# Performance work log

Measured on AMD Instinct MI355X. Metric: run time of the kernel, lower is better.

## Reference

```python
import jax, jax.numpy as jnp
import numpy as np
from jax import lax

C = 128
HEADS = 8
WS = 8
HIDDEN = C * 4


def _ln2d(x, w, b, eps=1e-6):
    # channel-first LayerNorm over dim 1 of [B,C,H,W]
    u = x.mean(axis=1, keepdims=True)
    s = ((x - u) ** 2).mean(axis=1, keepdims=True)
    xh = (x - u) / jnp.sqrt(s + eps)
    return w[None, :, None, None] * xh + b[None, :, None, None]


def _partition(x, ws):
    # [B,C,H,W] -> [B*nW, ws*ws, C]
    B, C_, H, W = x.shape
    x = x.transpose(0, 2, 3, 1)  # BHWC
    x = x.reshape(B, H // ws, ws, W // ws, ws, C_)
    x = x.transpose(0, 1, 3, 2, 4, 5)
    return x.reshape(-1, ws * ws, C_)


def _reverse(x, ws, H, W, B):
    # [B*nW, ws*ws, C] -> [B,C,H,W]
    C_ = x.shape[-1]
    x = x.reshape(B, H // ws, W // ws, ws, ws, C_)
    x = x.transpose(0, 1, 3, 2, 4, 5).reshape(B, H, W, C_)
    return x.transpose(0, 3, 1, 2)


def setup_inputs() -> dict:
    key = jax.random.key(0)
    ks = jax.random.split(key, 16)
    B, H, W = 4, 256, 256
    inp = {
        "x": jax.random.normal(ks[0], (B, C, H, W), jnp.float32),
        "l0": jax.random.uniform(ks[1], (B, 1, H, W), jnp.float32),
        "norm1_w": jnp.ones((C,), jnp.float32),
        "norm1_b": jnp.zeros((C,), jnp.float32),
        "norm2_w": jnp.ones((C,), jnp.float32),
        "norm2_b": jnp.zeros((C,), jnp.float32),
        "qkv_w": jax.random.normal(ks[2], (3 * C, C), jnp.float32) * (1.0 / np.sqrt(C)),
        "gate_w": jax.random.normal(ks[3], (C,), jnp.float32),
        "gate_b": jnp.zeros((C,), jnp.float32),
        "proj_w": jax.random.normal(ks[4], (C, C), jnp.float32) * (1.0 / np.sqrt(C)),
        "proj_b": jnp.zeros((C,), jnp.float32),
        "ffn_w1": jax.random.normal(ks[5], (HIDDEN, C), jnp.float32) * (1.0 / np.sqrt(C)),
        "ffn_b1": jnp.zeros((HIDDEN,), jnp.float32),
        "ffn_dw": jax.random.normal(ks[6], (HIDDEN, 1, 3, 3), jnp.float32) * (1.0 / 3.0),
        "ffn_dwb": jnp.zeros((HIDDEN,), jnp.float32),
        "ffn_w2": jax.random.normal(ks[7], (C, HIDDEN), jnp.float32) * (1.0 / np.sqrt(HIDDEN)),
        "ffn_b2": jnp.zeros((C,), jnp.float32),
    }
    return inp


def reference(x, l0, norm1_w, norm1_b, norm2_w, norm2_b, qkv_w, gate_w, gate_b,
              proj_w, proj_b, ffn_w1, ffn_b1, ffn_dw, ffn_dwb, ffn_w2, ffn_b2):
    B, C_, H, W = x.shape
    ws = WS
    # H,W chosen divisible by ws -> no padding branch
    head_dim = C_ // HEADS
    scale = head_dim ** -0.5

    shortcut = x
    xn = _ln2d(x, norm1_w, norm1_b)
    qkv = jnp.einsum("oc,bchw->bohw", qkv_w, xn)
    q, k, v = jnp.split(qkv, 3, axis=1)

    # illumination gate (l0 already at [H,W]; bilinear resize to same size is identity)
    gate = jax.nn.sigmoid(l0 * gate_w[None, :, None, None] + gate_b[None, :, None, None])
    q = q * gate

    q = _partition(q, ws)  # [Bw, ws*ws, C]
    k = _partition(k, ws)
    v = _partition(v, ws)
    Bw, N, _ = q.shape
    q = q.reshape(Bw, N, HEADS, head_dim)
    k = k.reshape(Bw, N, HEADS, head_dim)
    v = v.reshape(Bw, N, HEADS, head_dim)

    attn = jnp.einsum("bqhd,bkhd->bhqk", q, k) * scale
    attn = jax.nn.softmax(attn, axis=-1)
    out = jnp.einsum("bhqk,bkhd->bqhd", attn, v).reshape(Bw, N, C_)
    out = _reverse(out, ws, H, W, B)

    out = jnp.einsum("oc,bchw->bohw", proj_w, out) + proj_b[None, :, None, None]
    out = out + shortcut

    # FFN: 1x1 -> GELU -> depthwise 3x3 -> GELU -> 1x1
    h = _ln2d(out, norm2_w, norm2_b)
    h = jnp.einsum("oc,bchw->bohw", ffn_w1, h) + ffn_b1[None, :, None, None]
    h = jax.nn.gelu(h, approximate=False)
    h = lax.conv_general_dilated(h, ffn_dw, window_strides=(1, 1), padding="SAME",
                                 dimension_numbers=("NCHW", "OIHW", "NCHW"),
                                 feature_group_count=HIDDEN)
    h = h + ffn_dwb[None, :, None, None]
    h = jax.nn.gelu(h, approximate=False)
    h = jnp.einsum("oc,bchw->bohw", ffn_w2, h) + ffn_b2[None, :, None, None]
    return out + h
```

## Files before the change

### kernel.cpp

```cpp
#include <hip/hip_runtime.h>
#include <hip/hip_bf16.h>

#define HW   65536
#define CHW  (128*65536)
#define QKV_OZ  33554432u
#define QKV_H   1048576u
#define QKV_WIN 1024u

typedef __attribute__((ext_vector_type(8))) short bf16x8;
typedef __attribute__((ext_vector_type(4))) short bf16x4;
typedef __attribute__((ext_vector_type(4))) float f32x4;

__device__ __forceinline__ float geluf(float v){
    float u = 0.7978845608028654f * v * (1.f + 0.044715f*v*v);
    float e = __expf(2.f*u);
    float th = 1.f - 2.f/(e+1.f);
    return 0.5f*v*(1.f+th);
}

__device__ __forceinline__ float sigmoidf_(float z){
    return 1.f / (1.f + __expf(-z));
}

__device__ __forceinline__ float bf2f(short s){
    return __uint_as_float(((unsigned)(unsigned short)s) << 16);
}

__global__ __launch_bounds__(256) void k_cvt(
    const float* __restrict__ src, __hip_bfloat16* __restrict__ dst, int n)
{
    int i = blockIdx.x*256 + threadIdx.x;
    if (i < n) dst[i] = __float2bfloat16(src[i]);
}

__global__ __launch_bounds__(512,2) void k_ln_qkv_mfma(
    const float* __restrict__ x, const float* __restrict__ l0,
    const float* __restrict__ n1w, const float* __restrict__ n1b,
    const __hip_bfloat16* __restrict__ qkvw, const float* __restrict__ gate_w,
    const float* __restrict__ gate_b, __hip_bfloat16* __restrict__ qkvb)
{
    __shared__ short sxb[128*130];
    __shared__ float sp1[512], sp2[512];
    const int t = threadIdx.x;
    const int lane = t & 63, w = t >> 6;
    const int l15 = lane & 15, q4 = (lane >> 4)*4, ko = (lane >> 4)*8;
    const int mq = w & 3, phalf = w >> 2;
    const int pbase = blockIdx.x * 128;
    const int b = pbase >> 16;
    const int hw0 = pbase & 65535;
    const int x0 = hw0 & 255;
    const int y  = hw0 >> 8;
    const int wy = y >> 3, ty = y & 7;
    const int pxs = t & 127, cq = t >> 7;
    const float* xb = x + (size_t)b*CHW + (size_t)cq*32*HW + hw0 + pxs;
    unsigned* srow = (unsigned*)sxb + pxs*65 + cq*16;

    float s1 = 0.f, s2 = 0.f;
    #pragma unroll
    for (int j = 0; j < 16; ++j) {
        float v0 = xb[(size_t)(2*j)*HW];
        float v1 = xb[(size_t)(2*j+1)*HW];
        s1 += v0 + v1; s2 += v0*v0 + v1*v1;
        __hip_bfloat162 pk = __float22bfloat162_rn(make_float2(v0, v1));
        srow[j] = *(unsigned*)&pk;
    }
    sp1[cq*128 + pxs] = s1;
    sp2[cq*128 + pxs] = s2;
    __syncthreads();
    const float s1t = sp1[pxs] + sp1[128+pxs] + sp1[256+pxs] + sp1[384+pxs];
    const float s2t = sp2[pxs] + sp2[128+pxs] + sp2[256+pxs] + sp2[384+pxs];
    const float mean = s1t * 0.0078125f;
    const float rstd = rsqrtf(s2t*0.0078125f - mean*mean + 1e-6f);
    #pragma unroll
    for (int j = 0; j < 16; ++j) {
        unsigned u = srow[j];
        float v0 = __uint_as_float(u << 16);
        float v1 = __uint_as_float(u & 0xffff0000u);
        const int c = cq*32 + 2*j;
        v0 = (v0 - mean)*rstd*n1w[c]   + n1b[c];
        v1 = (v1 - mean)*rstd*n1w[c+1] + n1b[c+1];
        __hip_bfloat162 pk = __float22bfloat162_rn(make_float2(v0, v1));
        srow[j] = *(unsigned*)&pk;
    }
    __syncthreads();

    float lv[4];
    #pragma unroll
    for (int nt = 0; nt < 4; ++nt)
        lv[nt] = l0[(size_t)b*HW + hw0 + phalf*64 + nt*16 + l15];

    unsigned toff[4];
    #pragma unroll
    for (int nt = 0; nt < 4; ++nt) {
        const int xg = x0 + phalf*64 + nt*16 + l15;
        toff[nt] = (unsigned)((wy*32 + (xg >> 3))*1024 + (ty*8 + (xg & 7))*16);
    }

    const short* wq = (const short*)qkvw;
    for (int oz = 0; oz < 3; ++oz) {
        f32x4 acc[2][4];
        #pragma unroll
        for (int mt = 0; mt < 2; ++mt)
            #pragma unroll
            for (int nt = 0; nt < 4; ++nt)
                acc[mt][nt] = (f32x4){0.f,0.f,0.f,0.f};
        #pragma unroll
        for (int kc = 0; kc < 4; ++kc) {
            bf16x8 bfrag[4];
            #pragma unroll
            for (int nt = 0; nt < 4; ++nt) {
                const int px = phalf*64 + nt*16 + l15;
                bfrag[nt] = *(const bf16x8*)(sxb + px*130 + kc*32 + ko);
            }
            #pragma unroll
            for (int mt = 0; mt < 2; ++mt) {
                const int m = oz*128 + mq*32 + mt*16 + l15;
                bf16x8 af = *(const bf16x8*)(wq + m*128 + kc*32 + ko);
                #pragma unroll
                for (int nt = 0; nt < 4; ++nt)
                    acc[mt][nt] = __builtin_amdgcn_mfma_f32_16x16x32_bf16(af, bfrag[nt], acc[mt][nt], 0, 0, 0);
            }
        }
        __hip_bfloat16* ob = qkvb + (size_t)oz*QKV_OZ + (size_t)b*8*QKV_H;
        #pragma unroll
        for (int mt = 0; mt < 2; ++mt) {
            const int h = mq*2 + mt;
            #pragma unroll
            for (int nt = 0; nt < 4; ++nt) {
                float v0 = acc[mt][nt][0], v1 = acc[mt][nt][1];
                float v2 = acc[mt][nt][2], v3 = acc[mt][nt][3];
                if (oz == 0) {
                    const int o = h*16 + q4;
                    v0 *= sigmoidf_(lv[nt]*gate_w[o]   + gate_b[o]);
                    v1 *= sigmoidf_(lv[nt]*gate_w[o+1] + gate_b[o+1]);
                    v2 *= sigmoidf_(lv[nt]*gate_w[o+2] + gate_b[o+2]);
                    v3 *= sigmoidf_(lv[nt]*gate_w[o+3] + gate_b[o+3]);
                }
                __hip_bfloat162 p0 = __float22bfloat162_rn(make_float2(v0, v1));
                __hip_bfloat162 p1 = __float22bfloat162_rn(make_float2(v2, v3));
                uint2 st;
                st.x = *(unsigned*)&p0;
                st.y = *(unsigned*)&p1;
                *(uint2*)(ob + (size_t)h*QKV_H + toff[nt] + q4) = st;
            }
        }
    }
}

__global__ __launch_bounds__(256) void k_attn(
    const __hip_bfloat16* __restrict__ qkv, unsigned* __restrict__ apack)
{
    __shared__ short vt[4][16*72];
    __shared__ short pt[4][64*68];
    const int t = threadIdx.x;
    const int l = t & 63, w = t >> 6;
    const int c = l & 15, g = l >> 4;
    const int id = blockIdx.x*4 + w;
    const int b = id >> 13;
    const int head = (id >> 10) & 7;
    const int wi = id & 1023;
    const __hip_bfloat16* qp = qkv + ((size_t)(b*8 + head))*QKV_H + (size_t)wi*QKV_WIN;
    const __hip_bfloat16* kp = qp + QKV_OZ;
    const __hip_bfloat16* vp = qp + 2u*QKV_OZ;

    bf16x8 v0 = *(const bf16x8*)(vp + l*16);
    bf16x8 v1 = *(const bf16x8*)(vp + l*16 + 8);
    short* vtw = &vt[w][0];
    #pragma unroll
    for (int d = 0; d < 8; ++d) vtw[d*72 + l] = v0[d];
    #pragma unroll
    for (int d = 0; d < 8; ++d) vtw[(8+d)*72 + l] = v1[d];

    bf16x8 kf[4], qf[4];
    #pragma unroll
    for (int mj = 0; mj < 4; ++mj) {
        if (g < 2) {
            kf[mj] = *(const bf16x8*)(kp + (mj*16 + c)*16 + g*8);
            qf[mj] = *(const bf16x8*)(qp + (mj*16 + c)*16 + g*8);
        } else {
            kf[mj] = (bf16x8){0,0,0,0,0,0,0,0};
            qf[mj] = (bf16x8){0,0,0,0,0,0,0,0};
        }
    }
    f32x4 st[4][4];
    #pragma unroll
    for (int mj = 0; mj < 4; ++mj)
        #pragma unroll
        for (int ni = 0; ni < 4; ++ni)
            st[mj][ni] = (f32x4){0.f,0.f,0.f,0.f};
    #pragma unroll
    for (int mj = 0; mj < 4; ++mj)
        #pragma unroll
        for (int ni = 0; ni < 4; ++ni)
            st[mj][ni] = __builtin_amdgcn_mfma_f32_16x16x32_bf16(kf[mj], qf[ni], st[mj][ni], 0, 0, 0);

    float rs[4];
    bf16x4 pa[4][4], pb[4][4];
    #pragma unroll
    for (int ni = 0; ni < 4; ++ni) {
        float mx = -1e30f;
        #pragma unroll
        for (int mj = 0; mj < 4; ++mj)
            #pragma unroll
            for (int r = 0; r < 4; ++r)
                mx = fmaxf(mx, st[mj][ni][r]);
        mx = fmaxf(mx, __shfl_xor(mx, 16));
        mx = fmaxf(mx, __shfl_xor(mx, 32));
        mx *= 0.25f;
        float sum = 0.f;
        #pragma unroll
        for (int mj = 0; mj < 4; ++mj) {
            float p[4], lo[4];
            #pragma unroll
            for (int r = 0; r < 4; ++r) {
                p[r] = __expf(st[mj][ni][r]*0.25f - mx);
                sum += p[r];
            }
            __hip_bfloat162 h0 = __float22bfloat162_rn(make_float2(p[0], p[1]));
            __hip_bfloat162 h1 = __float22bfloat162_rn(make_float2(p[2], p[3]));
            union { unsigned u[2]; bf16x4 v; } hi;
            hi.u[0] = *(unsigned*)&h0; hi.u[1] = *(unsigned*)&h1;
            pa[mj][ni] = hi.v;
            #pragma unroll
            for (int r = 0; r < 4; ++r) lo[r] = p[r] - bf2f(hi.v[r]);
            __hip_bfloat162 g0 = __float22bfloat162_rn(make_float2(lo[0], lo[1]));
            __hip_bfloat162 g1 = __float22bfloat162_rn(make_float2(lo[2], lo[3]));
            union { unsigned u[2]; bf16x4 v; } lw;
            lw.u[0] = *(unsigned*)&g0; lw.u[1] = *(unsigned*)&g1;
            pb[mj][ni] = lw.v;
        }
        sum += __shfl_xor(sum, 16);
        sum += __shfl_xor(sum, 32);
        rs[ni] = 1.f / sum;
    }

    short* ptw = &pt[w][0];
    f32x4 oc[4];
    #pragma unroll
    for (int ni = 0; ni < 4; ++ni) oc[ni] = (f32x4){0.f,0.f,0.f,0.f};
    bf16x8 vf[2];
    #pragma unroll
    for (int kb = 0; kb < 2; ++kb)
        vf[kb] = *(const bf16x8*)(vtw + c*72 + kb*32 + g*8);

    #pragma unroll
    for (int mj = 0; mj < 4; ++mj)
        #pragma unroll
        for (int ni = 0; ni < 4; ++ni)
            *(bf16x4*)(ptw + (ni*16 + c)*68 + mj*16 + g*4) = pa[mj][ni];
    __syncthreads();
    #pragma unroll
    for (int kb = 0; kb < 2; ++kb)
        #pragma unroll
        for (int ni = 0; ni < 4; ++ni) {
            bf16x8 pf = *(const bf16x8*)(ptw + (ni*16 + c)*68 + kb*32 + g*8);
            oc[ni] = __builtin_amdgcn_mfma_f32_16x16x32_bf16(vf[kb], pf, oc[ni], 0, 0, 0);
        }
    __syncthreads();
    #pragma unroll
    for (int mj = 0; mj < 4; ++mj)
        #pragma unroll
        for (int ni = 0; ni < 4; ++ni)
            *(bf16x4*)(ptw + (ni*16 + c)*68 + mj*16 + g*4) = pb[mj][ni];
    __syncthreads();
    #pragma unroll
    for (int kb = 0; kb < 2; ++kb)
        #pragma unroll
        for (int ni = 0; ni < 4; ++ni) {
            bf16x8 pf = *(const bf16x8*)(ptw + (ni*16 + c)*68 + kb*32 + g*8);
            oc[ni] = __builtin_amdgcn_mfma_f32_16x16x32_bf16(vf[kb], pf, oc[ni], 0, 0, 0);
        }

    const int wy = wi >> 5, wx = wi & 31;
    unsigned* ob = apack + (size_t)b*64*HW + (size_t)(head*8 + g*2)*HW
                 + (size_t)(wy*8)*256 + wx*8;
    #pragma unroll
    for (int ni = 0; ni < 4; ++ni) {
        const int tok = ni*16 + c;
        const int hw = (tok >> 3)*256 + (tok & 7);
        __hip_bfloat162 p0 = __float22bfloat162_rn(make_float2(oc[ni][0]*rs[ni], oc[ni][1]*rs[ni]));
        __hip_bfloat162 p1 = __float22bfloat162_rn(make_float2(oc[ni][2]*rs[ni], oc[ni][3]*rs[ni]));
        ob[hw]            = *(unsigned*)&p0;
        ob[(size_t)HW+hw] = *(unsigned*)&p1;
    }
}

__global__ __launch_bounds__(256,3) void k_proj_mfma(
    const float* __restrict__ x, const unsigned* __restrict__ apack,
    const __hip_bfloat16* __restrict__ projw,
    const float* __restrict__ proj_b, float* __restrict__ out)
{
    __shared__ short sxb[128*130];
    const int t = threadIdx.x;
    const int lane = t & 63, w = t >> 6;
    const int l15 = lane & 15, q4 = (lane >> 4)*4, ko = (lane >> 4)*8;
    const int mhalf = w & 1, phalf = w >> 1;
    const int pbase = blockIdx.x * 128;
    const int b = pbase >> 16;
    const int hw0 = pbase & 65535;
    const int pxs = t & 127, chalf = t >> 7;
    const unsigned* hsrc = apack + (size_t)b*64*HW + (size_t)chalf*32*HW + hw0 + pxs;
    unsigned* sdst = (unsigned*)sxb + pxs*65 + chalf*32;
    #pragma unroll
    for (int c = 0; c < 32; ++c)
        sdst[c] = hsrc[(size_t)c*HW];
    __syncthreads();
    f32x4 acc[4][4];
    #pragma unroll
    for (int mt = 0; mt < 4; ++mt)
        #pragma unroll
        for (int nt = 0; nt < 4; ++nt)
            acc[mt][nt] = (f32x4){0.f,0.f,0.f,0.f};
    const short* wp = (const short*)projw;
    #pragma unroll
    for (int kc = 0; kc < 4; ++kc) {
        bf16x8 bfrag[4];
        #pragma unroll
        for (int nt = 0; nt < 4; ++nt) {
            const int px = phalf*64 + nt*16 + l15;
            bfrag[nt] = *(const bf16x8*)(sxb + px*130 + kc*32 + ko);
        }
        #pragma unroll
        for (int mt = 0; mt < 4; ++mt) {
            const int m = mhalf*64 + mt*16 + l15;
            bf16x8 af = *(const bf16x8*)(wp + m*128 + kc*32 + ko);
            #pragma unroll
            for (int nt = 0; nt < 4; ++nt)
                acc[mt][nt] = __builtin_amdgcn_mfma_f32_16x16x32_bf16(af, bfrag[nt], acc[mt][nt], 0, 0, 0);
        }
    }
    const float* xb = x + (size_t)b*CHW + hw0;
    float* ob = out + (size_t)b*CHW + hw0;
    #pragma unroll
    for (int mt = 0; mt < 4; ++mt)
        #pragma unroll
        for (int nt = 0; nt < 4; ++nt) {
            const int px = phalf*64 + nt*16 + l15;
            #pragma unroll
            for (int r = 0; r < 4; ++r) {
                const int o = mhalf*64 + mt*16 + q4 + r;
                ob[(size_t)o*HW + px] = acc[mt][nt][r] + proj_b[o] + xb[(size_t)o*HW + px];
            }
        }
}

__global__ __launch_bounds__(256,3) void k_ffn1_mfma(
    const float* __restrict__ outb2, const float* __restrict__ n2w, const float* __restrict__ n2b,
    const __hip_bfloat16* __restrict__ w1, const float* __restrict__ b1,
    __hip_bfloat16* __restrict__ h1s)
{
    __shared__ short sxb[128*130];
    __shared__ float sp1[256], sp2[256];
    const int t = threadIdx.x;
    const int lane = t & 63, w = t >> 6;
    const int l15 = lane & 15, q4 = (lane >> 4)*4, ko = (lane >> 4)*8;
    const int mhalf = w & 1, phalf = w >> 1;
    const int pbase = blockIdx.x * 128;
    const int b = pbase >> 16;
    const int hw0 = pbase & 65535;
    const int pxs = t & 127, chalf = t >> 7;
    const float* xb = outb2 + (size_t)b*CHW + (size_t)chalf*64*HW + hw0 + pxs;
    unsigned* srow = (unsigned*)sxb + pxs*65 + chalf*32;
    float s1 = 0.f, s2 = 0.f;
    #pragma unroll 8
    for (int j = 0; j < 32; ++j) {
        float v0 = xb[(size_t)(2*j)*HW];
        float v1 = xb[(size_t)(2*j+1)*HW];
        s1 += v0 + v1; s2 += v0*v0 + v1*v1;
        __hip_bfloat162 pk = __float22bfloat162_rn(make_float2(v0, v1));
        srow[j] = *(unsigned*)&pk;
    }
    sp1[chalf*128 + pxs] = s1;
    sp2[chalf*128 + pxs] = s2;
    __syncthreads();
    const float s1t = sp1[pxs] + sp1[128 + pxs];
    const float s2t = sp2[pxs] + sp2[128 + pxs];
    const float mean = s1t * 0.0078125f;
    const float rstd = rsqrtf(s2t*0.0078125f - mean*mean + 1e-6f);
    #pragma unroll 8
    for (int j = 0; j < 32; ++j) {
        unsigned u = srow[j];
        float v0 = __uint_as_float(u << 16);
        float v1 = __uint_as_float(u & 0xffff0000u);
        const int c = chalf*64 + 2*j;
        v0 = (v0 - mean)*rstd*n2w[c]   + n2b[c];
        v1 = (v1 - mean)*rstd*n2w[c+1] + n2b[c+1];
        __hip_bfloat162 pk = __float22bfloat162_rn(make_float2(v0, v1));
        srow[j] = *(unsigned*)&pk;
    }
    __syncthreads();
    const short* w1s = (const short*)w1;
    __hip_bfloat16* hb = h1s + (size_t)b*512*HW + hw0;
    for (int mc = 0; mc < 4; ++mc) {
        f32x4 acc[4][4];
        #pragma unroll
        for (int mt = 0; mt < 4; ++mt)
            #pragma unroll
            for (int nt = 0; nt < 4; ++nt)
                acc[mt][nt] = (f32x4){0.f,0.f,0.f,0.f};
        #pragma unroll
        for (int kc = 0; kc < 4; ++kc) {
            bf16x8 bfrag[4];
            #pragma unroll
            for (int nt = 0; nt < 4; ++nt) {
                const int px = phalf*64 + nt*16 + l15;
                bfrag[nt] = *(const bf16x8*)(sxb + px*130 + kc*32 + ko);
            }
            #pragma unroll
            for (int mt = 0; mt < 4; ++mt) {
                const int m = mc*128 + mhalf*64 + mt*16 + l15;
                bf16x8 af = *(const bf16x8*)(w1s + m*128 + kc*32 + ko);
                #pragma unroll
                for (int nt = 0; nt < 4; ++nt)
                    acc[mt][nt] = __builtin_amdgcn_mfma_f32_16x16x32_bf16(af, bfrag[nt], acc[mt][nt], 0, 0, 0);
            }
        }
        #pragma unroll
        for (int mt = 0; mt < 4; ++mt)
            #pragma unroll
            for (int nt = 0; nt < 4; ++nt) {
                const int px = phalf*64 + nt*16 + l15;
                #pragma unroll
                for (int r = 0; r < 4; ++r) {
                    const int o = mc*128 + mhalf*64 + mt*16 + q4 + r;
                    const float v = geluf(acc[mt][nt][r] + b1[o]);
                    hb[(size_t)o*HW + px] = __float2bfloat16(v);
                }
            }
    }
}

__global__ __launch_bounds__(256) void k_dwconv(
    const __hip_bfloat16* __restrict__ h1s,
    unsigned* __restrict__ h2u,
    const float* __restrict__ dwf, const float* __restrict__ dwb)
{
    __shared__ short sh[2*18*260];
    const int t = threadIdx.x;
    const int blk = blockIdx.x;
    const int b   = blk >> 12;
    const int rem = blk & 4095;
    const int rb = rem & 15;
    const int cp = rem >> 4;
    const int row0 = rb * 16;
    const __hip_bfloat16* h1b = h1s + (size_t)b*512*HW;
    #pragma unroll
    for (int ch = 0; ch < 2; ++ch) {
        const __hip_bfloat16* src = h1b + (size_t)(cp*2 + ch)*HW;
        #pragma unroll
        for (int i = 0; i < 9; ++i) {
            const int idx = t + i*256;
            const int r = idx >> 7;
            const int u = idx & 127;
            const int y = row0 - 1 + r;
            unsigned v = 0u;
            if ((unsigned)y < 256u) v = *(const unsigned*)(src + (size_t)y*256 + u*2);
            *(unsigned*)(&sh[ch*4680 + r*260 + 2 + u*2]) = v;
        }
    }
    if (t < 72) {
        const int ch = t / 36, q = t - ch*36;
        const int r = q >> 1;
        sh[ch*4680 + r*260 + ((q & 1) ? 258 : 1)] = 0;
    }
    __syncthreads();
    float wt[2][9], bs[2];
    #pragma unroll
    for (int ch = 0; ch < 2; ++ch) {
        const float* dwc = dwf + (size_t)(cp*2 + ch)*9;
        #pragma unroll
        for (int k = 0; k < 9; ++k) wt[ch][k] = dwc[k];
        bs[ch] = dwb[cp*2 + ch];
    }
    const int xp = (t & 127) * 2;
    const int rh = t >> 7;
    unsigned* h2b = h2u + (size_t)b*256*HW;
    #pragma unroll
    for (int r = 0; r < 8; ++r) {
        const int orow = rh*8 + r;
        const int y = row0 + orow;
        float res[2][2];
        #pragma unroll
        for (int ch = 0; ch < 2; ++ch) {
            const short* base = sh + ch*4680 + orow*260 + xp + 1;
            float a[3][4];
            #pragma unroll
            for (int dy = 0; dy < 3; ++dy)
                #pragma unroll
                for (int k = 0; k < 4; ++k)
                    a[dy][k] = __uint_as_float((unsigned)(unsigned short)base[dy*260 + k] << 16);
            #pragma unroll
            for (int xj = 0; xj < 2; ++xj) {
                float s = bs[ch];
                #pragma unroll
                for (int dy = 0; dy < 3; ++dy)
                    #pragma unroll
                    for (int dx = 0; dx < 3; ++dx)
                        s = fmaf(a[dy][xj+dx], wt[ch][dy*3+dx], s);
                res[ch][xj] = geluf(s);
            }
        }
        __hip_bfloat162 pk0 = __float22bfloat162_rn(make_float2(res[0][0], res[1][0]));
        __hip_bfloat162 pk1 = __float22bfloat162_rn(make_float2(res[0][1], res[1][1]));
        uint2 st;
        st.x = *(unsigned*)&pk0;
        st.y = *(unsigned*)&pk1;
        *(uint2*)(h2b + (size_t)cp*HW + (size_t)y*256 + xp) = st;
    }
}

__global__ __launch_bounds__(256,3) void k_ffn2g(
    const unsigned* __restrict__ h2u, const __hip_bfloat16* __restrict__ w2b,
    const float* __restrict__ b2, float* __restrict__ outb2)
{
    __shared__ short sxb[128*130];
    const int t = threadIdx.x;
    const int lane = t & 63, w = t >> 6;
    const int l15 = lane & 15, q4 = (lane >> 4)*4, ko = (lane >> 4)*8;
    const int mhalf = w & 1, phalf = w >> 1;
    const int pbase = blockIdx.x * 128;
    const int b = pbase >> 16;
    const int hw0 = pbase & 65535;
    const int pxs = t & 127;
    const int chalf = t >> 7;
    const unsigned* h2b = h2u + (size_t)b*256*HW;
    f32x4 acc[4][4];
    #pragma unroll
    for (int mt = 0; mt < 4; ++mt)
        #pragma unroll
        for (int nt = 0; nt < 4; ++nt)
            acc[mt][nt] = (f32x4){0.f,0.f,0.f,0.f};
    const short* w2s = (const short*)w2b;
    for (int k4 = 0; k4 < 4; ++k4) {
        if (k4) __syncthreads();
        const unsigned* hsrc = h2b + (size_t)(k4*64 + chalf*32)*HW + hw0 + pxs;
        unsigned* sdst = (unsigned*)sxb + pxs*65 + chalf*32;
        #pragma unroll
        for (int c = 0; c < 32; ++c)
            sdst[c] = hsrc[(size_t)c*HW];
        __syncthreads();
        #pragma unroll
        for (int kc = 0; kc < 4; ++kc) {
            bf16x8 bfrag[4];
            #pragma unroll
            for (int nt = 0; nt < 4; ++nt) {
                const int px = phalf*64 + nt*16 + l15;
                bfrag[nt] = *(const bf16x8*)(sxb + px*130 + kc*32 + ko);
            }
            #pragma unroll
            for (int mt = 0; mt < 4; ++mt) {
                const int m = mhalf*64 + mt*16 + l15;
                bf16x8 af = *(const bf16x8*)(w2s + (size_t)m*512 + k4*128 + kc*32 + ko);
                #pragma unroll
                for (int nt = 0; nt < 4; ++nt)
                    acc[mt][nt] = __builtin_amdgcn_mfma_f32_16x16x32_bf16(af, bfrag[nt], acc[mt][nt], 0, 0, 0);
            }
        }
    }
    float* ob = outb2 + (size_t)b*CHW;
    #pragma unroll
    for (int mt = 0; mt < 4; ++mt)
        #pragma unroll
        for (int nt = 0; nt < 4; ++nt) {
            const int px = hw0 + phalf*64 + nt*16 + l15;
            #pragma unroll
            for (int r = 0; r < 4; ++r) {
                const int o = mhalf*64 + mt*16 + q4 + r;
                ob[(size_t)o*HW + px] = acc[mt][nt][r] + b2[o] + ob[(size_t)o*HW + px];
            }
        }
}

extern "C" void kernel_launch(void* const* d_in, const int* in_sizes, int n_in,
                              void* d_out, int out_size, void* d_ws, size_t ws_size,
                              hipStream_t stream) {
    const float* x      = (const float*)d_in[0];
    const float* l0     = (const float*)d_in[1];
    const float* n1w    = (const float*)d_in[2];
    const float* n1b    = (const float*)d_in[3];
    const float* n2w    = (const float*)d_in[4];
    const float* n2b    = (const float*)d_in[5];
    const float* qkv_w  = (const float*)d_in[6];
    const float* gate_w = (const float*)d_in[7];
    const float* gate_b = (const float*)d_in[8];
    const float* proj_w = (const float*)d_in[9];
    const float* proj_b = (const float*)d_in[10];
    const float* ffn_w1 = (const float*)d_in[11];
    const float* ffn_b1 = (const float*)d_in[12];
    const float* ffn_dw = (const float*)d_in[13];
    const float* ffn_dwb= (const float*)d_in[14];
    const float* ffn_w2 = (const float*)d_in[15];
    const float* ffn_b2 = (const float*)d_in[16];

    float* out = (float*)d_out;
    __hip_bfloat16* qkvb = (__hip_bfloat16*)d_ws;
    unsigned* apack      = (unsigned*)((char*)d_ws + 201326592);
    __hip_bfloat16* h1s  = (__hip_bfloat16*)d_ws;
    unsigned* h2u        = (unsigned*)((char*)d_ws + 134217728);
    char* wbase = (char*)d_ws + 268435456;
    __hip_bfloat16* qkvw_b = (__hip_bfloat16*)(wbase);
    __hip_bfloat16* projw_b= (__hip_bfloat16*)(wbase + 98304);
    __hip_bfloat16* w1b    = (__hip_bfloat16*)(wbase + 131072);
    __hip_bfloat16* w2b    = (__hip_bfloat16*)(wbase + 262144);

    k_cvt<<<dim3(192), dim3(256), 0, stream>>>(qkv_w, qkvw_b, 49152);
    k_cvt<<<dim3(64),  dim3(256), 0, stream>>>(proj_w, projw_b, 16384);
    k_cvt<<<dim3(256), dim3(256), 0, stream>>>(ffn_w1, w1b, 65536);
    k_cvt<<<dim3(256), dim3(256), 0, stream>>>(ffn_w2, w2b, 65536);

    k_ln_qkv_mfma<<<dim3(2048), dim3(512), 0, stream>>>(x, l0, n1w, n1b, qkvw_b, gate_w, gate_b, qkvb);
    k_attn       <<<dim3(8192), dim3(256), 0, stream>>>(qkvb, apack);
    k_proj_mfma  <<<dim3(2048), dim3(256), 0, stream>>>(x, apack, projw_b, proj_b, out);
    for (int b2 = 0; b2 < 2; ++b2) {
        float* outp = out + (size_t)b2*2*CHW;
        k_ffn1_mfma<<<dim3(1024), dim3(256), 0, stream>>>(outp, n2w, n2b, w1b, ffn_b1, h1s);
        k_dwconv   <<<dim3(8192), dim3(256), 0, stream>>>(h1s, h2u, ffn_dw, ffn_dwb);
        k_ffn2g    <<<dim3(1024), dim3(256), 0, stream>>>(h2u, w2b, ffn_b2, outp);
    }
}
```

Baseline: 1.086 ms.

## Fuse depthwise conv and GELU into FFN second projection kernel

Removes the standalone depthwise 3x3 conv kernel and the h2 intermediate buffer. The new second-FFN kernel loads 16x16 spatial tiles with halo for 64 channels at a time into shared memory, computes the conv plus GELU, and feeds the result straight into the MFMA GEMM against w2. This avoids writing and re-reading the 512-channel bf16 intermediate through global memory, at the cost of halo re-reads, a larger shared-memory footprint and only 512 blocks per launch. Output writes now cover 16-pixel row segments instead of contiguous 128-pixel spans.

Measured after the change: 1.187 ms. 9.3% more time.

```diff
diff --git a/kernel.cpp b/kernel.cpp
--- a/kernel.cpp
+++ b/kernel.cpp
@@ -430,143 +430,121 @@
     }
 }
 
-__global__ __launch_bounds__(256) void k_dwconv(
-    const __hip_bfloat16* __restrict__ h1s,
-    unsigned* __restrict__ h2u,
-    const float* __restrict__ dwf, const float* __restrict__ dwb)
-{
-    __shared__ short sh[2*18*260];
-    const int t = threadIdx.x;
-    const int blk = blockIdx.x;
-    const int b   = blk >> 12;
-    const int rem = blk & 4095;
-    const int rb = rem & 15;
-    const int cp = rem >> 4;
-    const int row0 = rb * 16;
-    const __hip_bfloat16* h1b = h1s + (size_t)b*512*HW;
-    #pragma unroll
-    for (int ch = 0; ch < 2; ++ch) {
-        const __hip_bfloat16* src = h1b + (size_t)(cp*2 + ch)*HW;
-        #pragma unroll
-        for (int i = 0; i < 9; ++i) {
-            const int idx = t + i*256;
-            const int r = idx >> 7;
-            const int u = idx & 127;
-            const int y = row0 - 1 + r;
-            unsigned v = 0u;
-            if ((unsigned)y < 256u) v = *(const unsigned*)(src + (size_t)y*256 + u*2);
-            *(unsigned*)(&sh[ch*4680 + r*260 + 2 + u*2]) = v;
-        }
-    }
-    if (t < 72) {
-        const int ch = t / 36, q = t - ch*36;
-        const int r = q >> 1;
-        sh[ch*4680 + r*260 + ((q & 1) ? 258 : 1)] = 0;
-    }
-    __syncthreads();
-    float wt[2][9], bs[2];
-    #pragma unroll
-    for (int ch = 0; ch < 2; ++ch) {
-        const float* dwc = dwf + (size_t)(cp*2 + ch)*9;
-        #pragma unroll
-        for (int k = 0; k < 9; ++k) wt[ch][k] = dwc[k];
-        bs[ch] = dwb[cp*2 + ch];
-    }
-    const int xp = (t & 127) * 2;
-    const int rh = t >> 7;
-    unsigned* h2b = h2u + (size_t)b*256*HW;
-    #pragma unroll
-    for (int r = 0; r < 8; ++r) {
-        const int orow = rh*8 + r;
-        const int y = row0 + orow;
-        float res[2][2];
-        #pragma unroll
-        for (int ch = 0; ch < 2; ++ch) {
-            const short* base = sh + ch*4680 + orow*260 + xp + 1;
-            float a[3][4];
-            #pragma unroll
-            for (int dy = 0; dy < 3; ++dy)
-                #pragma unroll
-                for (int k = 0; k < 4; ++k)
-                    a[dy][k] = __uint_as_float((unsigned)(unsigned short)base[dy*260 + k] << 16);
-            #pragma unroll
-            for (int xj = 0; xj < 2; ++xj) {
-                float s = bs[ch];
-                #pragma unroll
-                for (int dy = 0; dy < 3; ++dy)
-                    #pragma unroll
-                    for (int dx = 0; dx < 3; ++dx)
-                        s = fmaf(a[dy][xj+dx], wt[ch][dy*3+dx], s);
-                res[ch][xj] = geluf(s);
-            }
-        }
-        __hip_bfloat162 pk0 = __float22bfloat162_rn(make_float2(res[0][0], res[1][0]));
-        __hip_bfloat162 pk1 = __float22bfloat162_rn(make_float2(res[0][1], res[1][1]));
-        uint2 st;
-        st.x = *(unsigned*)&pk0;
-        st.y = *(unsigned*)&pk1;
-        *(uint2*)(h2b + (size_t)cp*HW + (size_t)y*256 + xp) = st;
-    }
-}
-
-__global__ __launch_bounds__(256,3) void k_ffn2g(
-    const unsigned* __restrict__ h2u, const __hip_bfloat16* __restrict__ w2b,
+__global__ __launch_bounds__(512) void k_ffn2f(
+    const __hip_bfloat16* __restrict__ h1s, const __hip_bfloat16* __restrict__ w2b,
+    const float* __restrict__ dwf, const float* __restrict__ dwb,
     const float* __restrict__ b2, float* __restrict__ outb2)
 {
-    __shared__ short sxb[128*130];
+    __shared__ short sh1[64*370];
+    __shared__ short sconv[256*66];
     const int t = threadIdx.x;
-    const int lane = t & 63, w = t >> 6;
-    const int l15 = lane & 15, q4 = (lane >> 4)*4, ko = (lane >> 4)*8;
-    const int mhalf = w & 1, phalf = w >> 1;
-    const int pbase = blockIdx.x * 128;
-    const int b = pbase >> 16;
-    const int hw0 = pbase & 65535;
-    const int pxs = t & 127;
-    const int chalf = t >> 7;
-    const unsigned* h2b = h2u + (size_t)b*256*HW;
+    const int l = t & 63, w = t >> 6;
+    const int l15 = l & 15, q4 = (l >> 4)*4, ko = (l >> 4)*8;
+    const int mq2 = w & 1, pq = w >> 1;
+    const int b    = blockIdx.x >> 8;
+    const int tile = blockIdx.x & 255;
+    const int y0 = (tile >> 4) * 16;
+    const int x0 = (tile & 15) * 16;
+    const __hip_bfloat16* h1b = h1s + (size_t)b*512*HW;
+    const short* w2s = (const short*)w2b;
+
     f32x4 acc[4][4];
     #pragma unroll
     for (int mt = 0; mt < 4; ++mt)
         #pragma unroll
         for (int nt = 0; nt < 4; ++nt)
             acc[mt][nt] = (f32x4){0.f,0.f,0.f,0.f};
-    const short* w2s = (const short*)w2b;
-    for (int k4 = 0; k4 < 4; ++k4) {
-        if (k4) __syncthreads();
-        const unsigned* hsrc = h2b + (size_t)(k4*64 + chalf*32)*HW + hw0 + pxs;
-        unsigned* sdst = (unsigned*)sxb + pxs*65 + chalf*32;
-        #pragma unroll
-        for (int c = 0; c < 32; ++c)
-            sdst[c] = hsrc[(size_t)c*HW];
+
+    for (int ck = 0; ck < 8; ++ck) {
+        #pragma unroll
+        for (int i = 0; i < 23; ++i) {
+            const int idx = t + i*512;
+            if (idx < 11520) {
+                const int ch  = idx / 180;
+                const int rem = idx - ch*180;
+                const int r   = rem / 10;
+                const int u   = rem - r*10;
+                const int yy  = y0 - 1 + r;
+                const int cx  = x0 - 2 + u*2;
+                unsigned v = 0u;
+                if ((unsigned)yy < 256u && (unsigned)cx < 256u)
+                    v = *(const unsigned*)(h1b + (size_t)(ck*64 + ch)*HW + yy*256 + cx);
+                *(unsigned*)(&sh1[ch*370 + r*20 + u*2]) = v;
+            }
+        }
         __syncthreads();
-        #pragma unroll
-        for (int kc = 0; kc < 4; ++kc) {
+
+        float wt[9];
+        #pragma unroll
+        for (int k = 0; k < 9; ++k) wt[k] = dwf[(size_t)(ck*64 + l)*9 + k];
+        const float bsv = dwb[ck*64 + l];
+        const short* hrow = sh1 + l*370 + 2*w;
+        float a[3][6];
+        #pragma unroll
+        for (int rr = 0; rr < 3; ++rr) {
+            unsigned u0 = *(const unsigned*)(hrow + rr*20);
+            unsigned u1 = *(const unsigned*)(hrow + rr*20 + 2);
+            unsigned u2 = *(const unsigned*)(hrow + rr*20 + 4);
+            a[rr][0] = __uint_as_float(u0 << 16); a[rr][1] = __uint_as_float(u0 & 0xffff0000u);
+            a[rr][2] = __uint_as_float(u1 << 16); a[rr][3] = __uint_as_float(u1 & 0xffff0000u);
+            a[rr][4] = __uint_as_float(u2 << 16); a[rr][5] = __uint_as_float(u2 & 0xffff0000u);
+        }
+        #pragma unroll
+        for (int r = 0; r < 16; ++r) {
+            const int i0 = r % 3, i1 = (r+1) % 3, i2 = (r+2) % 3;
+            float s0 = bsv, s1v = bsv;
+            s0 = fmaf(a[i0][1], wt[0], s0); s0 = fmaf(a[i0][2], wt[1], s0); s0 = fmaf(a[i0][3], wt[2], s0);
+            s0 = fmaf(a[i1][1], wt[3], s0); s0 = fmaf(a[i1][2], wt[4], s0); s0 = fmaf(a[i1][3], wt[5], s0);
+            s0 = fmaf(a[i2][1], wt[6], s0); s0 = fmaf(a[i2][2], wt[7], s0); s0 = fmaf(a[i2][3], wt[8], s0);
+            s1v = fmaf(a[i0][2], wt[0], s1v); s1v = fmaf(a[i0][3], wt[1], s1v); s1v = fmaf(a[i0][4], wt[2], s1v);
+            s1v = fmaf(a[i1][2], wt[3], s1v); s1v = fmaf(a[i1][3], wt[4], s1v); s1v = fmaf(a[i1][4], wt[5], s1v);
+            s1v = fmaf(a[i2][2], wt[6], s1v); s1v = fmaf(a[i2][3], wt[7], s1v); s1v = fmaf(a[i2][4], wt[8], s1v);
+            const int px = r*16 + 2*w;
+            sconv[px*66 + l]       = (short)__bfloat16_as_short(__float2bfloat16(geluf(s0)));
+            sconv[(px+1)*66 + l]   = (short)__bfloat16_as_short(__float2bfloat16(geluf(s1v)));
+            if (r < 15) {
+                const int rr = r + 3;
+                unsigned u0 = *(const unsigned*)(hrow + rr*20);
+                unsigned u1 = *(const unsigned*)(hrow + rr*20 + 2);
+                unsigned u2 = *(const unsigned*)(hrow + rr*20 + 4);
+                a[i0][0] = __uint_as_float(u0 << 16); a[i0][1] = __uint_as_float(u0 & 0xffff0000u);
+                a[i0][2] = __uint_as_float(u1 << 16); a[i0][3] = __uint_as_float(u1 & 0xffff0000u);
+                a[i0][4] = __uint_as_float(u2 << 16); a[i0][5] = __uint_as_float(u2 & 0xffff0000u);
+            }
+        }
+        __syncthreads();
+
+        #pragma unroll
+        for (int kc = 0; kc < 2; ++kc) {
             bf16x8 bfrag[4];
             #pragma unroll
             for (int nt = 0; nt < 4; ++nt) {
-                const int px = phalf*64 + nt*16 + l15;
-                bfrag[nt] = *(const bf16x8*)(sxb + px*130 + kc*32 + ko);
+                const int px = pq*64 + nt*16 + l15;
+                bfrag[nt] = *(const bf16x8*)(sconv + px*66 + kc*32 + ko);
             }
             #pragma unroll
             for (int mt = 0; mt < 4; ++mt) {
-                const int m = mhalf*64 + mt*16 + l15;
-                bf16x8 af = *(const bf16x8*)(w2s + (size_t)m*512 + k4*128 + kc*32 + ko);
+                const int m = mq2*64 + mt*16 + l15;
+                bf16x8 af = *(const bf16x8*)(w2s + (size_t)m*512 + ck*64 + kc*32 + ko);
                 #pragma unroll
                 for (int nt = 0; nt < 4; ++nt)
                     acc[mt][nt] = __builtin_amdgcn_mfma_f32_16x16x32_bf16(af, bfrag[nt], acc[mt][nt], 0, 0, 0);
             }
         }
     }
+
     float* ob = outb2 + (size_t)b*CHW;
     #pragma unroll
     for (int mt = 0; mt < 4; ++mt)
         #pragma unroll
         for (int nt = 0; nt < 4; ++nt) {
-            const int px = hw0 + phalf*64 + nt*16 + l15;
+            const int px = pq*64 + nt*16 + l15;
+            const int row = px >> 4, col = px & 15;
             #pragma unroll
             for (int r = 0; r < 4; ++r) {
-                const int o = mhalf*64 + mt*16 + q4 + r;
-                ob[(size_t)o*HW + px] = acc[mt][nt][r] + b2[o] + ob[(size_t)o*HW + px];
+                const int o = mq2*64 + mt*16 + q4 + r;
+                const size_t off = (size_t)o*HW + (size_t)(y0+row)*256 + x0 + col;
+                ob[off] = acc[mt][nt][r] + b2[o] + ob[off];
             }
         }
 }
@@ -596,7 +574,6 @@
     __hip_bfloat16* qkvb = (__hip_bfloat16*)d_ws;
     unsigned* apack      = (unsigned*)((char*)d_ws + 201326592);
     __hip_bfloat16* h1s  = (__hip_bfloat16*)d_ws;
-    unsigned* h2u        = (unsigned*)((char*)d_ws + 134217728);
     char* wbase = (char*)d_ws + 268435456;
     __hip_bfloat16* qkvw_b = (__hip_bfloat16*)(wbase);
     __hip_bfloat16* projw_b= (__hip_bfloat16*)(wbase + 98304);
@@ -614,7 +591,6 @@
     for (int b2 = 0; b2 < 2; ++b2) {
         float* outp = out + (size_t)b2*2*CHW;
         k_ffn1_mfma<<<dim3(1024), dim3(256), 0, stream>>>(outp, n2w, n2b, w1b, ffn_b1, h1s);
-        k_dwconv   <<<dim3(8192), dim3(256), 0, stream>>>(h1s, h2u, ffn_dw, ffn_dwb);
-        k_ffn2g    <<<dim3(1024), dim3(256), 0, stream>>>(h2u, w2b, ffn_b2, outp);
-    }
-}
+        k_ffn2f    <<<dim3(512),  dim3(512), 0, stream>>>(h1s, w2b, ffn_dw, ffn_dwb, ffn_b2, outp);
+    }
+}
```
